# Performance work log

Hardware: AMD Instinct MI355X
Metric: run time of the kernel (lower is better)

The kernel has to match this reference:

```python
import jax, jax.numpy as jnp
import numpy as np
import math

B, S, D = 4, 4096, 256

def _linear(x, W, b):
    return jnp.einsum('bsd,ed->bse', x, W) + b

def _attn(x, Wq, bq, Wk, bk, Wv, bv, d):
    Q = _linear(x, Wq, bq)
    K = _linear(x, Wk, bk)
    V = _linear(x, Wv, bv)
    scores = jnp.einsum('bqd,bkd->bqk', Q, K) / math.sqrt(d)  # [B,S,S]
    w = jax.nn.softmax(scores, axis=-1)
    return jnp.einsum('bqk,bkd->bqd', w, V)

def setup_inputs() -> dict:
    key = jax.random.key(0)
    ks = jax.random.split(key, 32)
    p = {}
    p['x'] = jax.random.normal(ks[0], (B, S, D), dtype=jnp.float32)
    p['eps'] = jax.random.normal(ks[1], (B, S, D), dtype=jnp.float32)
    i = 2
    for name in ['Wq1','Wk1','Wv1','Wq2','Wk2','Wv2','Wmu','Wlv']:
        p[name] = 0.02 * jax.random.normal(ks[i], (D, D), dtype=jnp.float32); i += 1
    for name in ['bq1','bk1','bv1','bq2','bk2','bv2','bmu','blv']:
        p[name] = jnp.zeros((D,), dtype=jnp.float32)
    p['Wg'] = 0.02 * jax.random.normal(ks[i], (1, D), dtype=jnp.float32); i += 1
    p['bg'] = jnp.zeros((1,), dtype=jnp.float32)
    p['gamma'] = jnp.ones((D,), dtype=jnp.float32)
    p['beta'] = jnp.zeros((D,), dtype=jnp.float32)
    return p

def reference(x, eps, Wq1, Wk1, Wv1, Wq2, Wk2, Wv2, Wmu, Wlv,
              bq1, bk1, bv1, bq2, bk2, bv2, bmu, blv, Wg, bg, gamma, beta):
    d = x.shape[-1]
    h1 = _attn(x, Wq1, bq1, Wk1, bk1, Wv1, bv1, d)
    h2 = _attn(h1, Wq2, bq2, Wk2, bk2, Wv2, bv2, d)
    mu = _linear(h2, Wmu, bmu)
    logvar = _linear(h2, Wlv, blv)
    std = jnp.exp(0.5 * logvar)
    z = jax.nn.elu(mu + eps * std)
    p_gate = jax.nn.sigmoid(_linear(h2.mean(axis=1)[:, None, :], Wg, bg))[:, 0, 0]  # [B]
    y = x + z
    mean = y.mean(axis=-1, keepdims=True)
    var = y.var(axis=-1, keepdims=True)
    out = (y - mean) / jnp.sqrt(var + 1e-5) * gamma + beta
    return (out, mu, logvar, p_gate)
```

## Files before the change

### kernel.cpp

```cpp
#include <hip/hip_runtime.h>
#include <hip/hip_bf16.h>
#include <hip/hip_fp8.h>
#include <cstdint>
#include <cstddef>


#define S_LEN 4096
#define DMODEL 256
#define NBATCH 4
#define MTOT (NBATCH * S_LEN)

typedef __bf16 bf16;
typedef __bf16 bf16x8 __attribute__((ext_vector_type(8)));
typedef float f32x4 __attribute__((ext_vector_type(4)));
typedef float f32x16 __attribute__((ext_vector_type(16)));
typedef int i32x4 __attribute__((ext_vector_type(4)));
typedef int i32x8 __attribute__((ext_vector_type(8)));
typedef unsigned char u8;
typedef unsigned int u32;

__device__ __forceinline__ f32x4 mfma16(bf16x8 a, bf16x8 b, f32x4 c) {
  return __builtin_amdgcn_mfma_f32_16x16x32_bf16(a, b, c, 0, 0, 0);
}
__device__ __forceinline__ f32x16 mfma_mx(i32x8 a, i32x8 b, f32x16 c) {
  return __builtin_amdgcn_mfma_scale_f32_32x32x64_f8f6f4(
      a, b, c, 0 , 0 , 0, 0x7F7F7F7F, 0, 0x7F7F7F7F);
}

__device__ __forceinline__ void async16(const void* g, void* lds) {
  __builtin_amdgcn_global_load_lds(
      (const __attribute__((address_space(1))) unsigned int*)g,
      (__attribute__((address_space(3))) unsigned int*)lds, 16, 0, 0);
}

__device__ __forceinline__ unsigned short f2bfbits(float f) {
  return __builtin_bit_cast(unsigned short, (bf16)f);
}
__device__ __forceinline__ u8 f2fp8(float f) {
  __hip_fp8_e4m3 t(f);
  return *(u8*)&t;
}
__device__ __forceinline__ int permc(int v) {
  return (((v >> 5) & 1) << 7) + (((v >> 6) & 3) << 5) + (v & 31);
}
__device__ __forceinline__ int permc128(int v) {
  return (((v >> 5) & 1) << 6) + (((v >> 6) & 1) << 5) + (v & 31);
}

struct WPtrs { const float* p[8]; };

__global__ void cast_all_kernel(const f32x4* __restrict__ x, WPtrs wp,
                                ushort4* __restrict__ x16, ushort4* __restrict__ w16) {
  int bx = blockIdx.x, t = threadIdx.x;
  const f32x4* src;
  ushort4* dst;
  if (bx < 4096) {
    src = x + (size_t)bx * 256 + t;
    dst = x16 + (size_t)bx * 256 + t;
  } else {
    int r = bx - 4096;
    int m = r >> 6;
    int i = (r & 63) * 256 + t;
    src = (const f32x4*)wp.p[m] + i;
    dst = w16 + (size_t)m * 16384 + i;
  }
  f32x4 v = *src;
  ushort4 o;
  o.x = f2bfbits(v[0]); o.y = f2bfbits(v[1]); o.z = f2bfbits(v[2]); o.w = f2bfbits(v[3]);
  *dst = o;
}

struct GemmIO {
  const float* bias[3];
  void* out[3];
};

__global__ __launch_bounds__(256, 3) void gemm_qkv_kernel(const bf16* __restrict__ A,
                                                          const bf16* __restrict__ Wb,
                                                          GemmIO io) {
  __shared__ bf16 ldsA[128 * 64];
  __shared__ bf16 ldsB[128 * 64];
  const int t = threadIdx.x;
  const int m0 = blockIdx.x * 128;
  const int n0 = blockIdx.y * 128;
  const bf16* W = Wb + (size_t)blockIdx.z * 65536;
  const int w = t >> 6, l = t & 63, lm = l & 15, q = l >> 4;
  const int wr = (w >> 1) * 64, wc = (w & 1) * 64;

  f32x4 acc[4][4] = {};
#pragma unroll 1
  for (int it = 0; it < 4; ++it) {
    const int k0 = it * 64;
#pragma unroll
    for (int c = 0; c < 4; ++c) {
      int i = c * 256 + t;
      int r = i >> 3, c8 = (i & 7) ^ (r & 7);
      async16(A + (size_t)(m0 + r) * 256 + k0 + c8 * 8, &ldsA[i * 8]);
    }
#pragma unroll
    for (int c = 0; c < 4; ++c) {
      int i = c * 256 + t;
      int r = i >> 3, c8 = (i & 7) ^ (r & 7);
      async16(W + (size_t)(n0 + r) * 256 + k0 + c8 * 8, &ldsB[i * 8]);
    }
    __syncthreads();
#pragma unroll
    for (int ks = 0; ks < 2; ++ks) {
      bf16x8 af[4], bfr[4];
#pragma unroll
      for (int i = 0; i < 4; ++i) {
        int ra = wr + i * 16 + lm;
        af[i] = *(const bf16x8*)&ldsA[ra * 64 + ((((ks << 2) + q) ^ (ra & 7)) << 3)];
        int rb = wc + i * 16 + lm;
        bfr[i] = *(const bf16x8*)&ldsB[rb * 64 + ((((ks << 2) + q) ^ (rb & 7)) << 3)];
      }
#pragma unroll
      for (int i = 0; i < 4; ++i)
#pragma unroll
        for (int jj = 0; jj < 4; ++jj) acc[i][jj] = mfma16(af[i], bfr[jj], acc[i][jj]);
    }
    __syncthreads();
  }
  const float* bias = io.bias[blockIdx.z];
  if (blockIdx.z == 2) {
    bf16* out = (bf16*)io.out[2];
#pragma unroll
    for (int jj = 0; jj < 4; ++jj) {
      int col = n0 + wc + jj * 16 + lm;
      float bv = bias[col];
#pragma unroll
      for (int i = 0; i < 4; ++i) {
        int row = m0 + wr + i * 16 + q * 4;
#pragma unroll
        for (int r = 0; r < 4; ++r)
          out[(size_t)(row + r) * 256 + col] = (bf16)(acc[i][jj][r] + bv);
      }
    }
  } else {
    u8* out = (u8*)io.out[blockIdx.z];
#pragma unroll
    for (int jj = 0; jj < 4; ++jj) {
      int col = n0 + wc + jj * 16 + lm;
      int scol = (blockIdx.z == 1) ? permc(col) : col;
      float bv = bias[col];
#pragma unroll
      for (int i = 0; i < 4; ++i) {
        int row = m0 + wr + i * 16 + q * 4;
#pragma unroll
        for (int r = 0; r < 4; ++r)
          out[(size_t)(row + r) * 256 + scol] = f2fp8(acc[i][jj][r] + bv);
      }
    }
  }
}

__global__ __launch_bounds__(256, 3) void gemm_f_kernel(const bf16* __restrict__ A,
                                                        const bf16* __restrict__ Wb, GemmIO io) {
  __shared__ bf16 ldsA[128 * 64];
  __shared__ bf16 ldsB[128 * 64];
  const int t = threadIdx.x;
  const int m0 = blockIdx.x * 128;
  const int n0 = blockIdx.y * 128;
  const bf16* W = Wb + (size_t)blockIdx.z * 65536;
  const int w = t >> 6, l = t & 63, lm = l & 15, q = l >> 4;
  const int wr = (w >> 1) * 64, wc = (w & 1) * 64;

  f32x4 acc[4][4] = {};
#pragma unroll 1
  for (int it = 0; it < 4; ++it) {
    const int k0 = it * 64;
#pragma unroll
    for (int c = 0; c < 4; ++c) {
      int i = c * 256 + t;
      int r = i >> 3, c8 = (i & 7) ^ (r & 7);
      async16(A + (size_t)(m0 + r) * 256 + k0 + c8 * 8, &ldsA[i * 8]);
    }
#pragma unroll
    for (int c = 0; c < 4; ++c) {
      int i = c * 256 + t;
      int r = i >> 3, c8 = (i & 7) ^ (r & 7);
      async16(W + (size_t)(n0 + r) * 256 + k0 + c8 * 8, &ldsB[i * 8]);
    }
    __syncthreads();
#pragma unroll
    for (int ks = 0; ks < 2; ++ks) {
      bf16x8 af[4], bfr[4];
#pragma unroll
      for (int i = 0; i < 4; ++i) {
        int ra = wr + i * 16 + lm;
        af[i] = *(const bf16x8*)&ldsA[ra * 64 + ((((ks << 2) + q) ^ (ra & 7)) << 3)];
        int rb = wc + i * 16 + lm;
        bfr[i] = *(const bf16x8*)&ldsB[rb * 64 + ((((ks << 2) + q) ^ (rb & 7)) << 3)];
      }
#pragma unroll
      for (int i = 0; i < 4; ++i)
#pragma unroll
        for (int jj = 0; jj < 4; ++jj) acc[i][jj] = mfma16(af[i], bfr[jj], acc[i][jj]);
    }
    __syncthreads();
  }
  const float* bias = io.bias[blockIdx.z];
  float* out = (float*)io.out[blockIdx.z];
#pragma unroll
  for (int jj = 0; jj < 4; ++jj) {
    int col = n0 + wc + jj * 16 + lm;
    float bv = bias[col];
#pragma unroll
    for (int i = 0; i < 4; ++i) {
      int row = m0 + wr + i * 16 + q * 4;
#pragma unroll
      for (int r = 0; r < 4; ++r)
        out[(size_t)(row + r) * 256 + col] = acc[i][jj][r] + bv;
    }
  }
}

__global__ void transpose_kernel(const bf16* __restrict__ src, u8* __restrict__ dst) {
  __shared__ bf16 tile[64][72];
  int s0 = blockIdx.x * 64, d0 = blockIdx.y * 64;
  size_t boff = (size_t)blockIdx.z * S_LEN * 256;
  size_t boffT = (size_t)blockIdx.z * 256 * S_LEN;
  int t = threadIdx.x;
#pragma unroll
  for (int rep = 0; rep < 16; ++rep) {
    int lin = rep * 256 + t;
    int r = lin >> 6, c = lin & 63;
    tile[r][c] = src[boff + (size_t)(s0 + r) * 256 + d0 + c];
  }
  __syncthreads();
#pragma unroll
  for (int rep = 0; rep < 16; ++rep) {
    int lin = rep * 256 + t;
    int r = lin >> 6, c = lin & 63;
    int sg = s0 + c;
    int sp = (sg & ~127) + permc128(sg & 127);
    dst[boffT + (size_t)(d0 + r) * S_LEN + sp] = f2fp8((float)tile[c][r]);
  }
}

__global__ __launch_bounds__(1024, 4) void flash_kernel(const u8* __restrict__ Q,
                                                        const u8* __restrict__ K,
                                                        const u8* __restrict__ Vt,
                                                        bf16* __restrict__ O) {
  __shared__ __align__(16) u8 ldsK[2][128 * 256];
  __shared__ __align__(16) u8 ldsV[2][256 * 128];
  __shared__ __align__(16) u8 ldsP[2][2 * 32 * 128];
  __shared__ float lb[64];

  const int id = blockIdx.x;
  const int xcd = id & 7;
  const int b = xcd >> 1;
  const int qt = (id >> 3) + ((xcd & 1) << 5);

  const u8* Qb = Q + (size_t)b * S_LEN * 256;
  const u8* Kb = K + (size_t)b * S_LEN * 256;
  const u8* Vb = Vt + (size_t)b * 256 * S_LEN;
  bf16* Ob = O + (size_t)b * S_LEN * 256;

  const int t = threadIdx.x, w = t >> 6, lane = t & 63;
  const int m31 = lane & 31, kh = lane >> 5;
  const bool prod = (w < 8);
  const float CL2 = 0.09016844005556021f;

  if (t < 64) lb[t] = 0.f;

  int kld[2], kgo[2], vld[2], vgo[2];
#pragma unroll
  for (int it = 0; it < 2; ++it) {
    int c = it * 1024 + t;
    kld[it] = c * 16;
    int kr = c >> 4, kg2 = (c & 15) ^ (kr & 7);
    kgo[it] = kr * 256 + kg2 * 16;
    vld[it] = c * 16;
    int vr = c >> 3, vg2 = (c & 7) ^ (vr & 7);
    vgo[it] = vr * S_LEN + vg2 * 16;
  }

  const int qg = w & 1, ks = (w >> 1) & 3;
  const int kn = ks * 32 + m31;
  const int kx = kn & 7;
  const int px = m31 & 7;
  i32x8 qf[4];
  if (prod) {
    const u8* qrow = Qb + (size_t)(qt * 64 + qg * 32 + m31) * 256 + kh * 32;
#pragma unroll
    for (int b2 = 0; b2 < 4; ++b2) qf[b2] = *(const i32x8*)(qrow + b2 * 64);
  }
  const int cw = w - 8;
  const int cqg = cw & 1, dpair = cw >> 1;
  const int vd0 = dpair * 64 + m31;
  const int vx = vd0 & 7;

  f32x16 o0 = {}, o1 = {};
  float l_w = 0.f;

#pragma unroll
  for (int it = 0; it < 2; ++it) async16(Kb + kgo[it], &ldsK[0][kld[it]]);
  __syncthreads();

#pragma unroll 1
  for (int j = 0; j <= 32; ++j) {
    if (j < 32) {
      const u8* vg = Vb + j * 128;
#pragma unroll
      for (int it = 0; it < 2; ++it) async16(vg + vgo[it], &ldsV[j & 1][vld[it]]);
    }
    if (j < 31) {
      const u8* kg = Kb + (size_t)(j + 1) * 128 * 256;
#pragma unroll
      for (int it = 0; it < 2; ++it) async16(kg + kgo[it], &ldsK[(j + 1) & 1][kld[it]]);
    }
    if (prod) {
      if (j < 32) {
        const u8* kb = &ldsK[j & 1][kn * 256 + kh * 128];
        f32x16 s = {};
        __builtin_amdgcn_s_setprio(1);
#pragma unroll
        for (int b2 = 0; b2 < 4; ++b2) {
          i32x4 klo = *(const i32x4*)(kb + (((2 * b2) ^ kx) << 4));
          i32x4 khi = *(const i32x4*)(kb + (((2 * b2 + 1) ^ kx) << 4));
          s = mfma_mx(__builtin_shufflevector(klo, khi, 0, 1, 2, 3, 4, 5, 6, 7), qf[b2], s);
        }
        __builtin_amdgcn_s_setprio(0);
        float p[16];
#pragma unroll
        for (int r = 0; r < 16; ++r) {
          p[r] = __builtin_amdgcn_exp2f(s[r] * CL2);
          l_w += p[r];
        }
        u8* pst = &ldsP[j & 1][qg * 4096 + m31 * 128 + 4 * kh];
        const int cb = (ks & 1) * 4 + (ks >> 1) * 2;
#pragma unroll
        for (int g2 = 0; g2 < 4; ++g2) {
          int pk = __builtin_amdgcn_cvt_pk_fp8_f32(p[4 * g2], p[4 * g2 + 1], 0, false);
          pk = __builtin_amdgcn_cvt_pk_fp8_f32(p[4 * g2 + 2], p[4 * g2 + 3], pk, true);
          *(u32*)(pst + (((cb + (g2 >> 1)) ^ px) << 4) + ((g2 & 1) << 3)) = (u32)pk;
        }
      }
    } else {
      if (j > 0) {
        const int pb = (j - 1) & 1;
        const u8* pr = &ldsP[pb][cqg * 4096 + m31 * 128];
        const u8* v0 = &ldsV[pb][(size_t)vd0 * 128];
        const u8* v1 = v0 + 32 * 128;
        __builtin_amdgcn_s_setprio(1);
#pragma unroll
        for (int b2 = 0; b2 < 2; ++b2) {
          const int ca = 4 * kh + 2 * b2;
          i32x4 plo = *(const i32x4*)(pr + ((ca ^ px) << 4));
          i32x4 phi = *(const i32x4*)(pr + (((ca + 1) ^ px) << 4));
          i32x8 pa = __builtin_shufflevector(plo, phi, 0, 1, 2, 3, 4, 5, 6, 7);
          i32x4 va = *(const i32x4*)(v0 + ((ca ^ vx) << 4));
          i32x4 vb2 = *(const i32x4*)(v0 + (((ca + 1) ^ vx) << 4));
          o0 = mfma_mx(pa, __builtin_shufflevector(va, vb2, 0, 1, 2, 3, 4, 5, 6, 7), o0);
          i32x4 vc = *(const i32x4*)(v1 + ((ca ^ vx) << 4));
          i32x4 vd2 = *(const i32x4*)(v1 + (((ca + 1) ^ vx) << 4));
          o1 = mfma_mx(pa, __builtin_shufflevector(vc, vd2, 0, 1, 2, 3, 4, 5, 6, 7), o1);
        }
        __builtin_amdgcn_s_setprio(0);
      }
    }
    __syncthreads();
  }

  if (prod) {
    l_w += __shfl_xor(l_w, 32, 64);
    if (kh == 0) atomicAdd(&lb[qg * 32 + m31], l_w);
  }
  __syncthreads();

  if (!prod) {
    bf16* ob0 = Ob + (size_t)(qt * 64 + cqg * 32) * 256 + dpair * 64;
#pragma unroll
    for (int reg = 0; reg < 16; ++reg) {
      const int row = (reg & 3) + 8 * (reg >> 2) + 4 * kh;
      float li = lb[cqg * 32 + row];
      ob0[(size_t)row * 256 + m31] = (bf16)(o0[reg] / li);
      ob0[(size_t)row * 256 + 32 + m31] = (bf16)(o1[reg] / li);
    }
  }
}

__global__ __launch_bounds__(256) void gate_partial(const bf16* __restrict__ h,
                                                    float* __restrict__ part) {
  int bb = blockIdx.y;
  const bf16* hb = h + (size_t)bb * S_LEN * 256 + (size_t)blockIdx.x * 64 * 256;
  int t = threadIdx.x;
  float acc = 0.f;
#pragma unroll 4
  for (int s = 0; s < 64; ++s) acc += (float)hb[s * 256 + t];
  part[((size_t)bb * 64 + blockIdx.x) * 256 + t] = acc;
}

__global__ __launch_bounds__(256) void gate_final(const float* __restrict__ part,
                                                  const float* __restrict__ Wg,
                                                  const float* __restrict__ bg,
                                                  float* __restrict__ pg) {
  int bb = blockIdx.x, t = threadIdx.x;
  const float* p = part + (size_t)bb * 64 * 256;
  float acc = 0.f;
#pragma unroll 4
  for (int c = 0; c < 64; ++c) acc += p[c * 256 + t];
  acc *= Wg[t] * (1.0f / 4096.0f);
  __shared__ float red[256];
  red[t] = acc;
  __syncthreads();
  if (t < 64) {
    float a = red[t] + red[t + 64] + red[t + 128] + red[t + 192];
#pragma unroll
    for (int d = 1; d < 64; d <<= 1) a += __shfl_xor(a, d, 64);
    if (t == 0) pg[bb] = 1.0f / (1.0f + __expf(-(a + bg[0])));
  }
}

__global__ __launch_bounds__(256) void epilogue_kernel(const float* __restrict__ x,
                                                       const float* __restrict__ eps,
                                                       const float* __restrict__ mu,
                                                       const float* __restrict__ lv,
                                                       const float* __restrict__ gamma,
                                                       const float* __restrict__ beta,
                                                       float* __restrict__ out) {
  size_t base = (size_t)blockIdx.x * 1024 + (threadIdx.x >> 6) * 256;
  int l = threadIdx.x & 63;
  f32x4 xv = ((const f32x4*)(x + base))[l];
  f32x4 ev = ((const f32x4*)(eps + base))[l];
  f32x4 mv = ((const f32x4*)(mu + base))[l];
  f32x4 vv = ((const f32x4*)(lv + base))[l];
  f32x4 y;
  float s = 0.f, s2 = 0.f;
#pragma unroll
  for (int c = 0; c < 4; ++c) {
    float z = mv[c] + ev[c] * __expf(0.5f * vv[c]);
    z = z > 0.f ? z : (__expf(z) - 1.f);
    float yy = xv[c] + z;
    y[c] = yy;
    s += yy;
    s2 += yy * yy;
  }
#pragma unroll
  for (int d = 1; d < 64; d <<= 1) {
    s += __shfl_xor(s, d, 64);
    s2 += __shfl_xor(s2, d, 64);
  }
  float mean = s * (1.f / 256.f);
  float var = s2 * (1.f / 256.f) - mean * mean;
  float rstd = rsqrtf(var + 1e-5f);
  f32x4 gv = ((const f32x4*)gamma)[l];
  f32x4 bv = ((const f32x4*)beta)[l];
  f32x4 o;
#pragma unroll
  for (int c = 0; c < 4; ++c) o[c] = (y[c] - mean) * rstd * gv[c] + bv[c];
  ((f32x4*)(out + base))[l] = o;
}

extern "C" void kernel_launch(void* const* d_in, const int* in_sizes, int n_in, void* d_out,
                              int out_size, void* d_ws, size_t ws_size, hipStream_t stream) {
  const float* x = (const float*)d_in[0];
  const float* eps = (const float*)d_in[1];
  const float* Wg = (const float*)d_in[18];
  const float* bg = (const float*)d_in[19];
  const float* gamma = (const float*)d_in[20];
  const float* beta = (const float*)d_in[21];

  char* ws = (char*)d_ws;
  bf16* x16 = (bf16*)(ws);
  bf16* h16 = (bf16*)(ws + 8388608);
  bf16* v16 = (bf16*)(ws + 16777216);
  u8* q8 = (u8*)(ws + 25165824);
  u8* k8 = (u8*)(ws + 29360128);
  u8* vt8 = (u8*)(ws + 33554432);
  bf16* w16 = (bf16*)(ws + 37748736);
  float* gpart = (float*)(ws + 38797312);

  float* out = (float*)d_out;
  float* mu = out + 4194304;
  float* lv = out + 8388608;
  float* pg = out + 12582912;

  WPtrs wp;
  for (int i = 0; i < 8; ++i) wp.p[i] = (const float*)d_in[2 + i];
  cast_all_kernel<<<4608, 256, 0, stream>>>((const f32x4*)x, wp, (ushort4*)x16, (ushort4*)w16);

  GemmIO io1;
  io1.bias[0] = (const float*)d_in[10];
  io1.bias[1] = (const float*)d_in[11];
  io1.bias[2] = (const float*)d_in[12];
  io1.out[0] = q8; io1.out[1] = k8; io1.out[2] = v16;
  gemm_qkv_kernel<<<dim3(128, 2, 3), 256, 0, stream>>>(x16, w16, io1);
  transpose_kernel<<<dim3(64, 4, 4), 256, 0, stream>>>(v16, vt8);
  flash_kernel<<<256, 1024, 0, stream>>>(q8, k8, vt8, h16);

  GemmIO io2;
  io2.bias[0] = (const float*)d_in[13];
  io2.bias[1] = (const float*)d_in[14];
  io2.bias[2] = (const float*)d_in[15];
  io2.out[0] = q8; io2.out[1] = k8; io2.out[2] = v16;
  gemm_qkv_kernel<<<dim3(128, 2, 3), 256, 0, stream>>>(h16, w16 + 3 * 65536, io2);
  transpose_kernel<<<dim3(64, 4, 4), 256, 0, stream>>>(v16, vt8);
  flash_kernel<<<256, 1024, 0, stream>>>(q8, k8, vt8, h16);

  GemmIO io3;
  io3.bias[0] = (const float*)d_in[16];
  io3.bias[1] = (const float*)d_in[17];
  io3.bias[2] = nullptr;
  io3.out[0] = mu; io3.out[1] = lv; io3.out[2] = nullptr;
  gemm_f_kernel<<<dim3(128, 2, 2), 256, 0, stream>>>(h16, w16 + 6 * 65536, io3);

  gate_partial<<<dim3(64, 4), 256, 0, stream>>>(h16, gpart);
  gate_final<<<4, 256, 0, stream>>>(gpart, Wg, bg, pg);
  epilogue_kernel<<<4096, 256, 0, stream>>>(x, eps, mu, lv, gamma, beta, out);
}
```

Measured before the change: 298.2 us.

## Fuse V transpose into QKV GEMM and restructure flash producer/consumer pipeline

The V projection GEMM now writes fp8 V directly in a blocked, permuted transposed layout, which removes the separate transpose kernel and the bf16 V round trip. The flash kernel drops its LDS staging of V: consumer warps load their V fragments straight from global memory into registers, one tile ahead. K is kept in a triple-buffered LDS ring that the consumer warps fill. The loop becomes an explicitly software-pipelined schedule with raw s_barrier calls and manual waitcnts in place of __syncthreads. This frees LDS and cuts per-iteration barrier cost, but it relies on the global V loads being hidden behind compute and on the hand-placed waits being correct.

Result: slower. 495.5 us (+66.2%).

```diff
diff --git a/kernel.cpp b/kernel.cpp
--- a/kernel.cpp
+++ b/kernel.cpp
@@ -8,7 +8,6 @@
 #define S_LEN 4096
 #define DMODEL 256
 #define NBATCH 4
-#define MTOT (NBATCH * S_LEN)
 
 typedef __bf16 bf16;
 typedef __bf16 bf16x8 __attribute__((ext_vector_type(8)));
@@ -24,7 +23,10 @@
 }
 __device__ __forceinline__ f32x16 mfma_mx(i32x8 a, i32x8 b, f32x16 c) {
   return __builtin_amdgcn_mfma_scale_f32_32x32x64_f8f6f4(
-      a, b, c, 0 , 0 , 0, 0x7F7F7F7F, 0, 0x7F7F7F7F);
+      a, b, c, 0, 0, 0, 0x7F7F7F7F, 0, 0x7F7F7F7F);
+}
+__device__ __forceinline__ i32x8 cat8(i32x4 a, i32x4 b) {
+  return __builtin_shufflevector(a, b, 0, 1, 2, 3, 4, 5, 6, 7);
 }
 
 __device__ __forceinline__ void async16(const void* g, void* lds) {
@@ -123,7 +125,7 @@
   }
   const float* bias = io.bias[blockIdx.z];
   if (blockIdx.z == 2) {
-    bf16* out = (bf16*)io.out[2];
+    u8* out = (u8*)io.out[2];
 #pragma unroll
     for (int jj = 0; jj < 4; ++jj) {
       int col = n0 + wc + jj * 16 + lm;
@@ -132,8 +134,12 @@
       for (int i = 0; i < 4; ++i) {
         int row = m0 + wr + i * 16 + q * 4;
 #pragma unroll
-        for (int r = 0; r < 4; ++r)
-          out[(size_t)(row + r) * 256 + col] = (bf16)(acc[i][jj][r] + bv);
+        for (int r = 0; r < 4; ++r) {
+          int rg = row + r;
+          int bb = rg >> 12, s = rg & 4095;
+          out[(((size_t)(bb * 32 + (s >> 7)) * 256 + col) << 7) + permc128(s & 127)] =
+              f2fp8(acc[i][jj][r] + bv);
+        }
       }
     }
   } else {
@@ -215,35 +221,11 @@
   }
 }
 
-__global__ void transpose_kernel(const bf16* __restrict__ src, u8* __restrict__ dst) {
-  __shared__ bf16 tile[64][72];
-  int s0 = blockIdx.x * 64, d0 = blockIdx.y * 64;
-  size_t boff = (size_t)blockIdx.z * S_LEN * 256;
-  size_t boffT = (size_t)blockIdx.z * 256 * S_LEN;
-  int t = threadIdx.x;
-#pragma unroll
-  for (int rep = 0; rep < 16; ++rep) {
-    int lin = rep * 256 + t;
-    int r = lin >> 6, c = lin & 63;
-    tile[r][c] = src[boff + (size_t)(s0 + r) * 256 + d0 + c];
-  }
-  __syncthreads();
-#pragma unroll
-  for (int rep = 0; rep < 16; ++rep) {
-    int lin = rep * 256 + t;
-    int r = lin >> 6, c = lin & 63;
-    int sg = s0 + c;
-    int sp = (sg & ~127) + permc128(sg & 127);
-    dst[boffT + (size_t)(d0 + r) * S_LEN + sp] = f2fp8((float)tile[c][r]);
-  }
-}
-
 __global__ __launch_bounds__(1024, 4) void flash_kernel(const u8* __restrict__ Q,
                                                         const u8* __restrict__ K,
                                                         const u8* __restrict__ Vt,
                                                         bf16* __restrict__ O) {
-  __shared__ __align__(16) u8 ldsK[2][128 * 256];
-  __shared__ __align__(16) u8 ldsV[2][256 * 128];
+  __shared__ __align__(16) u8 ldsK[3][32768];
   __shared__ __align__(16) u8 ldsP[2][2 * 32 * 128];
   __shared__ float lb[64];
 
@@ -254,7 +236,7 @@
 
   const u8* Qb = Q + (size_t)b * S_LEN * 256;
   const u8* Kb = K + (size_t)b * S_LEN * 256;
-  const u8* Vb = Vt + (size_t)b * 256 * S_LEN;
+  const u8* Vb = Vt + (size_t)b * 1048576;
   bf16* Ob = O + (size_t)b * S_LEN * 256;
 
   const int t = threadIdx.x, w = t >> 6, lane = t & 63;
@@ -263,18 +245,6 @@
   const float CL2 = 0.09016844005556021f;
 
   if (t < 64) lb[t] = 0.f;
-
-  int kld[2], kgo[2], vld[2], vgo[2];
-#pragma unroll
-  for (int it = 0; it < 2; ++it) {
-    int c = it * 1024 + t;
-    kld[it] = c * 16;
-    int kr = c >> 4, kg2 = (c & 15) ^ (kr & 7);
-    kgo[it] = kr * 256 + kg2 * 16;
-    vld[it] = c * 16;
-    int vr = c >> 3, vg2 = (c & 7) ^ (vr & 7);
-    vgo[it] = vr * S_LEN + vg2 * 16;
-  }
 
   const int qg = w & 1, ks = (w >> 1) & 3;
   const int kn = ks * 32 + m31;
@@ -286,99 +256,127 @@
 #pragma unroll
     for (int b2 = 0; b2 < 4; ++b2) qf[b2] = *(const i32x8*)(qrow + b2 * 64);
   }
+  float l_w = 0.f;
+
   const int cw = w - 8;
   const int cqg = cw & 1, dpair = cw >> 1;
   const int vd0 = dpair * 64 + m31;
-  const int vx = vd0 & 7;
-
+  const int ct = (t - 512) & 511;
   f32x16 o0 = {}, o1 = {};
-  float l_w = 0.f;
-
-#pragma unroll
-  for (int it = 0; it < 2; ++it) async16(Kb + kgo[it], &ldsK[0][kld[it]]);
-  __syncthreads();
+  i32x4 vA[8];
+
+  auto STAGE = [&](int m) {
+    const u8* kg = Kb + (size_t)m * 32768;
+    u8* kd = ldsK[m % 3];
+#pragma unroll
+    for (int jj = 0; jj < 4; ++jj) {
+      int c = jj * 512 + ct;
+      int kr = c >> 4, g = (c & 15) ^ (kr & 7);
+      async16(kg + kr * 256 + g * 16, kd + c * 16);
+    }
+  };
+  auto CONSV = [&](int m) {
+    const u8* vt = Vb + (size_t)m * 32768 + (size_t)vd0 * 128 + kh * 64;
+    vA[0] = *(const i32x4*)(vt);
+    vA[1] = *(const i32x4*)(vt + 16);
+    vA[2] = *(const i32x4*)(vt + 32);
+    vA[3] = *(const i32x4*)(vt + 48);
+    vA[4] = *(const i32x4*)(vt + 4096);
+    vA[5] = *(const i32x4*)(vt + 4112);
+    vA[6] = *(const i32x4*)(vt + 4128);
+    vA[7] = *(const i32x4*)(vt + 4144);
+  };
+  auto PROD = [&](int i) {
+    const u8* kb = &ldsK[i % 3][kn * 256 + kh * 128];
+    f32x16 s = {};
+    __builtin_amdgcn_s_setprio(1);
+#pragma unroll
+    for (int b2 = 0; b2 < 4; ++b2) {
+      i32x4 clo = *(const i32x4*)(kb + (((2 * b2) ^ kx) << 4));
+      i32x4 chi = *(const i32x4*)(kb + (((2 * b2 + 1) ^ kx) << 4));
+      s = mfma_mx(cat8(clo, chi), qf[b2], s);
+    }
+    __builtin_amdgcn_s_setprio(0);
+    u8* pst = &ldsP[i & 1][qg * 4096 + m31 * 128 + 4 * kh];
+    const int cb = (ks & 1) * 4 + (ks >> 1) * 2;
+#pragma unroll
+    for (int g2 = 0; g2 < 4; ++g2) {
+      float p0 = __builtin_amdgcn_exp2f(s[4 * g2] * CL2);
+      float p1 = __builtin_amdgcn_exp2f(s[4 * g2 + 1] * CL2);
+      float p2 = __builtin_amdgcn_exp2f(s[4 * g2 + 2] * CL2);
+      float p3 = __builtin_amdgcn_exp2f(s[4 * g2 + 3] * CL2);
+      l_w += (p0 + p1) + (p2 + p3);
+      int pk = __builtin_amdgcn_cvt_pk_fp8_f32(p0, p1, 0, false);
+      pk = __builtin_amdgcn_cvt_pk_fp8_f32(p2, p3, pk, true);
+      *(u32*)(pst + (((cb + (g2 >> 1)) ^ px) << 4) + ((g2 & 1) << 3)) = (u32)pk;
+    }
+  };
+  auto PV = [&](int i) {
+    const u8* pr = &ldsP[i & 1][cqg * 4096 + m31 * 128];
+    __builtin_amdgcn_s_setprio(1);
+#pragma unroll
+    for (int b2 = 0; b2 < 2; ++b2) {
+      const int ca = 4 * kh + 2 * b2;
+      i32x4 plo = *(const i32x4*)(pr + ((ca ^ px) << 4));
+      i32x4 phi = *(const i32x4*)(pr + (((ca + 1) ^ px) << 4));
+      i32x8 pa = cat8(plo, phi);
+      o0 = mfma_mx(pa, cat8(vA[2 * b2], vA[2 * b2 + 1]), o0);
+      o1 = mfma_mx(pa, cat8(vA[4 + 2 * b2], vA[5 + 2 * b2]), o1);
+    }
+    __builtin_amdgcn_s_setprio(0);
+  };
+
+#define BARRIER() do { __builtin_amdgcn_s_barrier(); asm volatile("" ::: "memory"); } while (0)
+#define PWAIT() asm volatile("s_waitcnt lgkmcnt(0)" ::: "memory")
+
+#pragma unroll
+  for (int rep = 0; rep < 4; ++rep) {
+    int c = rep * 1024 + t;
+    int tile = c >> 11, cc = c & 2047;
+    int kr = cc >> 4, g = (cc & 15) ^ (kr & 7);
+    async16(Kb + tile * 32768 + kr * 256 + g * 16, &ldsK[tile][cc * 16]);
+  }
+  asm volatile("s_waitcnt vmcnt(0) lgkmcnt(0)" ::: "memory");
+  BARRIER();
+
+  if (prod) { PROD(0); PWAIT(); }
+  else { STAGE(2); CONSV(0); }
+  BARRIER();
 
 #pragma unroll 1
-  for (int j = 0; j <= 32; ++j) {
-    if (j < 32) {
-      const u8* vg = Vb + j * 128;
-#pragma unroll
-      for (int it = 0; it < 2; ++it) async16(vg + vgo[it], &ldsV[j & 1][vld[it]]);
-    }
-    if (j < 31) {
-      const u8* kg = Kb + (size_t)(j + 1) * 128 * 256;
-#pragma unroll
-      for (int it = 0; it < 2; ++it) async16(kg + kgo[it], &ldsK[(j + 1) & 1][kld[it]]);
-    }
-    if (prod) {
-      if (j < 32) {
-        const u8* kb = &ldsK[j & 1][kn * 256 + kh * 128];
-        f32x16 s = {};
-        __builtin_amdgcn_s_setprio(1);
-#pragma unroll
-        for (int b2 = 0; b2 < 4; ++b2) {
-          i32x4 klo = *(const i32x4*)(kb + (((2 * b2) ^ kx) << 4));
-          i32x4 khi = *(const i32x4*)(kb + (((2 * b2 + 1) ^ kx) << 4));
-          s = mfma_mx(__builtin_shufflevector(klo, khi, 0, 1, 2, 3, 4, 5, 6, 7), qf[b2], s);
-        }
-        __builtin_amdgcn_s_setprio(0);
-        float p[16];
-#pragma unroll
-        for (int r = 0; r < 16; ++r) {
-          p[r] = __builtin_amdgcn_exp2f(s[r] * CL2);
-          l_w += p[r];
-        }
-        u8* pst = &ldsP[j & 1][qg * 4096 + m31 * 128 + 4 * kh];
-        const int cb = (ks & 1) * 4 + (ks >> 1) * 2;
-#pragma unroll
-        for (int g2 = 0; g2 < 4; ++g2) {
-          int pk = __builtin_amdgcn_cvt_pk_fp8_f32(p[4 * g2], p[4 * g2 + 1], 0, false);
-          pk = __builtin_amdgcn_cvt_pk_fp8_f32(p[4 * g2 + 2], p[4 * g2 + 3], pk, true);
-          *(u32*)(pst + (((cb + (g2 >> 1)) ^ px) << 4) + ((g2 & 1) << 3)) = (u32)pk;
-        }
-      }
-    } else {
-      if (j > 0) {
-        const int pb = (j - 1) & 1;
-        const u8* pr = &ldsP[pb][cqg * 4096 + m31 * 128];
-        const u8* v0 = &ldsV[pb][(size_t)vd0 * 128];
-        const u8* v1 = v0 + 32 * 128;
-        __builtin_amdgcn_s_setprio(1);
-#pragma unroll
-        for (int b2 = 0; b2 < 2; ++b2) {
-          const int ca = 4 * kh + 2 * b2;
-          i32x4 plo = *(const i32x4*)(pr + ((ca ^ px) << 4));
-          i32x4 phi = *(const i32x4*)(pr + (((ca + 1) ^ px) << 4));
-          i32x8 pa = __builtin_shufflevector(plo, phi, 0, 1, 2, 3, 4, 5, 6, 7);
-          i32x4 va = *(const i32x4*)(v0 + ((ca ^ vx) << 4));
-          i32x4 vb2 = *(const i32x4*)(v0 + (((ca + 1) ^ vx) << 4));
-          o0 = mfma_mx(pa, __builtin_shufflevector(va, vb2, 0, 1, 2, 3, 4, 5, 6, 7), o0);
-          i32x4 vc = *(const i32x4*)(v1 + ((ca ^ vx) << 4));
-          i32x4 vd2 = *(const i32x4*)(v1 + (((ca + 1) ^ vx) << 4));
-          o1 = mfma_mx(pa, __builtin_shufflevector(vc, vd2, 0, 1, 2, 3, 4, 5, 6, 7), o1);
-        }
-        __builtin_amdgcn_s_setprio(0);
-      }
-    }
-    __syncthreads();
-  }
+  for (int j = 1; j <= 29; ++j) {
+    if (prod) { PROD(j); PWAIT(); }
+    else { STAGE(j + 2); PV(j - 1); CONSV(j); }
+    BARRIER();
+  }
+
+  if (prod) { PROD(30); PWAIT(); }
+  else { PV(29); CONSV(30); }
+  BARRIER();
+  if (prod) { PROD(31); PWAIT(); }
+  else { PV(30); CONSV(31); }
+  BARRIER();
 
   if (prod) {
     l_w += __shfl_xor(l_w, 32, 64);
     if (kh == 0) atomicAdd(&lb[qg * 32 + m31], l_w);
+  } else {
+    PV(31);
   }
   __syncthreads();
 
   if (!prod) {
-    bf16* ob0 = Ob + (size_t)(qt * 64 + cqg * 32) * 256 + dpair * 64;
+    bf16* ob = Ob + (size_t)(qt * 64 + cqg * 32) * 256 + dpair * 64;
 #pragma unroll
     for (int reg = 0; reg < 16; ++reg) {
       const int row = (reg & 3) + 8 * (reg >> 2) + 4 * kh;
       float li = lb[cqg * 32 + row];
-      ob0[(size_t)row * 256 + m31] = (bf16)(o0[reg] / li);
-      ob0[(size_t)row * 256 + 32 + m31] = (bf16)(o1[reg] / li);
-    }
-  }
+      ob[(size_t)row * 256 + m31] = (bf16)(o0[reg] / li);
+      ob[(size_t)row * 256 + 32 + m31] = (bf16)(o1[reg] / li);
+    }
+  }
+#undef BARRIER
+#undef PWAIT
 }
 
 __global__ __launch_bounds__(256) void gate_partial(const bf16* __restrict__ h,
@@ -465,7 +463,6 @@
   char* ws = (char*)d_ws;
   bf16* x16 = (bf16*)(ws);
   bf16* h16 = (bf16*)(ws + 8388608);
-  bf16* v16 = (bf16*)(ws + 16777216);
   u8* q8 = (u8*)(ws + 25165824);
   u8* k8 = (u8*)(ws + 29360128);
   u8* vt8 = (u8*)(ws + 33554432);
@@ -485,18 +482,16 @@
   io1.bias[0] = (const float*)d_in[10];
   io1.bias[1] = (const float*)d_in[11];
   io1.bias[2] = (const float*)d_in[12];
-  io1.out[0] = q8; io1.out[1] = k8; io1.out[2] = v16;
+  io1.out[0] = q8; io1.out[1] = k8; io1.out[2] = vt8;
   gemm_qkv_kernel<<<dim3(128, 2, 3), 256, 0, stream>>>(x16, w16, io1);
-  transpose_kernel<<<dim3(64, 4, 4), 256, 0, stream>>>(v16, vt8);
   flash_kernel<<<256, 1024, 0, stream>>>(q8, k8, vt8, h16);
 
   GemmIO io2;
   io2.bias[0] = (const float*)d_in[13];
   io2.bias[1] = (const float*)d_in[14];
   io2.bias[2] = (const float*)d_in[15];
-  io2.out[0] = q8; io2.out[1] = k8; io2.out[2] = v16;
+  io2.out[0] = q8; io2.out[1] = k8; io2.out[2] = vt8;
   gemm_qkv_kernel<<<dim3(128, 2, 3), 256, 0, stream>>>(h16, w16 + 3 * 65536, io2);
-  transpose_kernel<<<dim3(64, 4, 4), 256, 0, stream>>>(v16, vt8);
   flash_kernel<<<256, 1024, 0, stream>>>(q8, k8, vt8, h16);
 
   GemmIO io3;
```

## Fuse V transpose and fp8 cast into QKV GEMM epilogue with tiled V layout

Applied to the files above, without the earlier changes.

The QKV GEMM epilogue for V now converts to fp8 and stages a transposed 128-row tile in shared memory, then writes it with 16-byte stores into a new tiled V^T layout of 256x128 blocks. The separate transpose kernel and the bf16 V buffer are removed in both attention layers. The flash kernel's V addressing is changed to read contiguous 32 KB tiles per key block. This removes two kernel launches and an extra bf16 round trip through global memory, at the cost of an extra barrier and shared-memory staging in the GEMM epilogue.

Measured after the change: 280.0 us. -6.1%, faster.

```diff
diff --git a/kernel.cpp b/kernel.cpp
--- a/kernel.cpp
+++ b/kernel.cpp
@@ -8,7 +8,6 @@
 #define S_LEN 4096
 #define DMODEL 256
 #define NBATCH 4
-#define MTOT (NBATCH * S_LEN)
 
 typedef __bf16 bf16;
 typedef __bf16 bf16x8 __attribute__((ext_vector_type(8)));
@@ -24,7 +23,10 @@
 }
 __device__ __forceinline__ f32x16 mfma_mx(i32x8 a, i32x8 b, f32x16 c) {
   return __builtin_amdgcn_mfma_scale_f32_32x32x64_f8f6f4(
-      a, b, c, 0 , 0 , 0, 0x7F7F7F7F, 0, 0x7F7F7F7F);
+      a, b, c, 0, 0, 0, 0x7F7F7F7F, 0, 0x7F7F7F7F);
+}
+__device__ __forceinline__ i32x8 cat8(i32x4 a, i32x4 b) {
+  return __builtin_shufflevector(a, b, 0, 1, 2, 3, 4, 5, 6, 7);
 }
 
 __device__ __forceinline__ void async16(const void* g, void* lds) {
@@ -78,8 +80,8 @@
 __global__ __launch_bounds__(256, 3) void gemm_qkv_kernel(const bf16* __restrict__ A,
                                                           const bf16* __restrict__ Wb,
                                                           GemmIO io) {
-  __shared__ bf16 ldsA[128 * 64];
-  __shared__ bf16 ldsB[128 * 64];
+  __shared__ __align__(16) bf16 ldsA[128 * 64];
+  __shared__ __align__(16) bf16 ldsB[128 * 64];
   const int t = threadIdx.x;
   const int m0 = blockIdx.x * 128;
   const int n0 = blockIdx.y * 128;
@@ -123,18 +125,26 @@
   }
   const float* bias = io.bias[blockIdx.z];
   if (blockIdx.z == 2) {
-    bf16* out = (bf16*)io.out[2];
+    u8* vstage = (u8*)ldsA;
 #pragma unroll
     for (int jj = 0; jj < 4; ++jj) {
-      int col = n0 + wc + jj * 16 + lm;
-      float bv = bias[col];
+      int dloc = wc + jj * 16 + lm;
+      float bv = bias[n0 + dloc];
 #pragma unroll
       for (int i = 0; i < 4; ++i) {
-        int row = m0 + wr + i * 16 + q * 4;
-#pragma unroll
-        for (int r = 0; r < 4; ++r)
-          out[(size_t)(row + r) * 256 + col] = (bf16)(acc[i][jj][r] + bv);
-      }
+        int kvb = wr + i * 16 + q * 4;
+        u32 word = (u32)f2fp8(acc[i][jj][0] + bv) | ((u32)f2fp8(acc[i][jj][1] + bv) << 8) |
+                   ((u32)f2fp8(acc[i][jj][2] + bv) << 16) | ((u32)f2fp8(acc[i][jj][3] + bv) << 24);
+        *(u32*)&vstage[dloc * 128 + permc128(kvb)] = word;
+      }
+    }
+    __syncthreads();
+    int gtile = (m0 >> 12) * 32 + ((m0 & 4095) >> 7);
+    u8* outb = (u8*)io.out[2] + ((size_t)gtile * 256 + n0) * 128;
+#pragma unroll
+    for (int cidx = 0; cidx < 4; ++cidx) {
+      int c = cidx * 256 + t;
+      ((i32x4*)outb)[c] = ((const i32x4*)vstage)[c];
     }
   } else {
     u8* out = (u8*)io.out[blockIdx.z];
@@ -215,29 +225,6 @@
   }
 }
 
-__global__ void transpose_kernel(const bf16* __restrict__ src, u8* __restrict__ dst) {
-  __shared__ bf16 tile[64][72];
-  int s0 = blockIdx.x * 64, d0 = blockIdx.y * 64;
-  size_t boff = (size_t)blockIdx.z * S_LEN * 256;
-  size_t boffT = (size_t)blockIdx.z * 256 * S_LEN;
-  int t = threadIdx.x;
-#pragma unroll
-  for (int rep = 0; rep < 16; ++rep) {
-    int lin = rep * 256 + t;
-    int r = lin >> 6, c = lin & 63;
-    tile[r][c] = src[boff + (size_t)(s0 + r) * 256 + d0 + c];
-  }
-  __syncthreads();
-#pragma unroll
-  for (int rep = 0; rep < 16; ++rep) {
-    int lin = rep * 256 + t;
-    int r = lin >> 6, c = lin & 63;
-    int sg = s0 + c;
-    int sp = (sg & ~127) + permc128(sg & 127);
-    dst[boffT + (size_t)(d0 + r) * S_LEN + sp] = f2fp8((float)tile[c][r]);
-  }
-}
-
 __global__ __launch_bounds__(1024, 4) void flash_kernel(const u8* __restrict__ Q,
                                                         const u8* __restrict__ K,
                                                         const u8* __restrict__ Vt,
@@ -254,7 +241,7 @@
 
   const u8* Qb = Q + (size_t)b * S_LEN * 256;
   const u8* Kb = K + (size_t)b * S_LEN * 256;
-  const u8* Vb = Vt + (size_t)b * 256 * S_LEN;
+  const u8* Vb = Vt + (size_t)b * 1048576;
   bf16* Ob = O + (size_t)b * S_LEN * 256;
 
   const int t = threadIdx.x, w = t >> 6, lane = t & 63;
@@ -273,7 +260,7 @@
     kgo[it] = kr * 256 + kg2 * 16;
     vld[it] = c * 16;
     int vr = c >> 3, vg2 = (c & 7) ^ (vr & 7);
-    vgo[it] = vr * S_LEN + vg2 * 16;
+    vgo[it] = vr * 128 + vg2 * 16;
   }
 
   const int qg = w & 1, ks = (w >> 1) & 3;
@@ -301,7 +288,7 @@
 #pragma unroll 1
   for (int j = 0; j <= 32; ++j) {
     if (j < 32) {
-      const u8* vg = Vb + j * 128;
+      const u8* vg = Vb + (size_t)j * 32768;
 #pragma unroll
       for (int it = 0; it < 2; ++it) async16(vg + vgo[it], &ldsV[j & 1][vld[it]]);
     }
@@ -319,7 +306,7 @@
         for (int b2 = 0; b2 < 4; ++b2) {
           i32x4 klo = *(const i32x4*)(kb + (((2 * b2) ^ kx) << 4));
           i32x4 khi = *(const i32x4*)(kb + (((2 * b2 + 1) ^ kx) << 4));
-          s = mfma_mx(__builtin_shufflevector(klo, khi, 0, 1, 2, 3, 4, 5, 6, 7), qf[b2], s);
+          s = mfma_mx(cat8(klo, khi), qf[b2], s);
         }
         __builtin_amdgcn_s_setprio(0);
         float p[16];
@@ -349,13 +336,13 @@
           const int ca = 4 * kh + 2 * b2;
           i32x4 plo = *(const i32x4*)(pr + ((ca ^ px) << 4));
           i32x4 phi = *(const i32x4*)(pr + (((ca + 1) ^ px) << 4));
-          i32x8 pa = __builtin_shufflevector(plo, phi, 0, 1, 2, 3, 4, 5, 6, 7);
+          i32x8 pa = cat8(plo, phi);
           i32x4 va = *(const i32x4*)(v0 + ((ca ^ vx) << 4));
           i32x4 vb2 = *(const i32x4*)(v0 + (((ca + 1) ^ vx) << 4));
-          o0 = mfma_mx(pa, __builtin_shufflevector(va, vb2, 0, 1, 2, 3, 4, 5, 6, 7), o0);
+          o0 = mfma_mx(pa, cat8(va, vb2), o0);
           i32x4 vc = *(const i32x4*)(v1 + ((ca ^ vx) << 4));
           i32x4 vd2 = *(const i32x4*)(v1 + (((ca + 1) ^ vx) << 4));
-          o1 = mfma_mx(pa, __builtin_shufflevector(vc, vd2, 0, 1, 2, 3, 4, 5, 6, 7), o1);
+          o1 = mfma_mx(pa, cat8(vc, vd2), o1);
         }
         __builtin_amdgcn_s_setprio(0);
       }
@@ -465,7 +452,6 @@
   char* ws = (char*)d_ws;
   bf16* x16 = (bf16*)(ws);
   bf16* h16 = (bf16*)(ws + 8388608);
-  bf16* v16 = (bf16*)(ws + 16777216);
   u8* q8 = (u8*)(ws + 25165824);
   u8* k8 = (u8*)(ws + 29360128);
   u8* vt8 = (u8*)(ws + 33554432);
@@ -485,18 +471,16 @@
   io1.bias[0] = (const float*)d_in[10];
   io1.bias[1] = (const float*)d_in[11];
   io1.bias[2] = (const float*)d_in[12];
-  io1.out[0] = q8; io1.out[1] = k8; io1.out[2] = v16;
+  io1.out[0] = q8; io1.out[1] = k8; io1.out[2] = vt8;
   gemm_qkv_kernel<<<dim3(128, 2, 3), 256, 0, stream>>>(x16, w16, io1);
-  transpose_kernel<<<dim3(64, 4, 4), 256, 0, stream>>>(v16, vt8);
   flash_kernel<<<256, 1024, 0, stream>>>(q8, k8, vt8, h16);
 
   GemmIO io2;
   io2.bias[0] = (const float*)d_in[13];
   io2.bias[1] = (const float*)d_in[14];
   io2.bias[2] = (const float*)d_in[15];
-  io2.out[0] = q8; io2.out[1] = k8; io2.out[2] = v16;
+  io2.out[0] = q8; io2.out[1] = k8; io2.out[2] = vt8;
   gemm_qkv_kernel<<<dim3(128, 2, 3), 256, 0, stream>>>(h16, w16 + 3 * 65536, io2);
-  transpose_kernel<<<dim3(64, 4, 4), 256, 0, stream>>>(v16, vt8);
   flash_kernel<<<256, 1024, 0, stream>>>(q8, k8, vt8, h16);
 
   GemmIO io3;
```
